# Kernel tuning notes

Hardware: AMD Instinct MI355X
Metric: run time of the kernel (lower is better)

Reference implementation:

```python
import jax, jax.numpy as jnp
import numpy as np

BATCH = 1024
INPUT_DIM = 4096
HIDDEN_DIM = 4096
N_BLOCKS = 8
BLOCK_SIZE = HIDDEN_DIM // N_BLOCKS          # 512
IN_BLOCK_SIZE = INPUT_DIM // N_BLOCKS        # 512


def setup_inputs() -> dict:
    key = jax.random.key(0)
    ks = jax.random.split(key, 6)
    scale = 1.0 / np.sqrt(BLOCK_SIZE)  # torch GRUCell init: U(-1/sqrt(hidden), 1/sqrt(hidden))
    return {
        "x": jax.random.normal(ks[0], (BATCH, INPUT_DIM), dtype=jnp.float32),
        "h": jax.random.normal(ks[1], (BATCH, HIDDEN_DIM), dtype=jnp.float32),
        "W_ih": jax.random.normal(ks[2], (N_BLOCKS, 3 * BLOCK_SIZE, IN_BLOCK_SIZE), dtype=jnp.float32) * scale,
        "W_hh": jax.random.normal(ks[3], (N_BLOCKS, 3 * BLOCK_SIZE, BLOCK_SIZE), dtype=jnp.float32) * scale,
        "b_ih": jax.random.normal(ks[4], (N_BLOCKS, 3 * BLOCK_SIZE), dtype=jnp.float32) * scale,
        "b_hh": jax.random.normal(ks[5], (N_BLOCKS, 3 * BLOCK_SIZE), dtype=jnp.float32) * scale,
    }


def reference(x, h, W_ih, W_hh, b_ih, b_hh):
    B = x.shape[0]
    n, g3, ibs = W_ih.shape           # n_blocks, 3*block_size, input_block_size
    bs = W_hh.shape[2]                # block_size
    xb = x.reshape(B, n, ibs)         # (B, n_blocks, input_block_size)
    hb = h.reshape(B, n, bs)          # (B, n_blocks, block_size)
    # Block-diagonal GEMM: one grouped matmul over all blocks at once.
    gi = jnp.einsum('bni,ngi->bng', xb, W_ih) + b_ih   # (B, n, 3*bs)
    gh = jnp.einsum('bnh,ngh->bng', hb, W_hh) + b_hh   # (B, n, 3*bs)
    i_r, i_z, i_n = jnp.split(gi, 3, axis=-1)
    h_r, h_z, h_n = jnp.split(gh, 3, axis=-1)
    r = jax.nn.sigmoid(i_r + h_r)                      # reset gate
    z = jax.nn.sigmoid(i_z + h_z)                      # update gate
    n_gate = jnp.tanh(i_n + r * h_n)                   # candidate state
    new_h = n_gate + z * (hb - n_gate)                 # torch GRUCell: h' = (1-z)*n + z*h
    return new_h.reshape(B, n * bs)
```

## Files before the change

kernel.cpp:

```cpp
#include <hip/hip_runtime.h>
#include <hip/hip_bf16.h>
#include <stdint.h>

#define G1CAST(p) ((const __attribute__((address_space(1))) void*)(p))
#define L3CAST(p) ((__attribute__((address_space(3))) void*)(p))

typedef short bf16x8 __attribute__((ext_vector_type(8)));
typedef float f32x16 __attribute__((ext_vector_type(16)));

static __device__ __forceinline__ short f2bf(float f) {
    __hip_bfloat16 b = __float2bfloat16(f);
    return __builtin_bit_cast(short, b);
}

__global__ __launch_bounds__(256) void wconv_kernel(const float* __restrict__ Wih,
                                                    const float* __restrict__ Whh,
                                                    short* __restrict__ Wstep) {
    const int b = blockIdx.x;
    const int vb = (b & 7) * 768 + (b >> 3);
    const int gid = vb * 256 + threadIdx.x;
    const int lane = gid & 63;
    int t1 = gid >> 6;
    const int g = t1 % 3;  t1 /= 3;
    const int wn = t1 & 1; t1 >>= 1;
    const int s = t1 & 63; t1 >>= 6;
    const int jt = t1 & 7;
    const int nblk = t1 >> 3;
    const int j = jt * 64 + wn * 32 + (lane & 31);
    const int kk = s * 16 + (lane >> 5) * 8;
    const float* src = (kk < 512)
        ? Wih + ((int64_t)nblk * 786432 + (int64_t)(g * 512 + j) * 512 + kk)
        : Whh + ((int64_t)nblk * 786432 + (int64_t)(g * 512 + j) * 512 + (kk - 512));
    const float4 a = ((const float4*)src)[0];
    const float4 bq = ((const float4*)src)[1];
    bf16x8 o;
    o[0] = f2bf(a.x); o[1] = f2bf(a.y); o[2] = f2bf(a.z); o[3] = f2bf(a.w);
    o[4] = f2bf(bq.x); o[5] = f2bf(bq.y); o[6] = f2bf(bq.z); o[7] = f2bf(bq.w);
    *(bf16x8*)(Wstep + (size_t)gid * 8) = o;
}

__global__ __launch_bounds__(256) void aconv_kernel(const float* __restrict__ x,
                                                    const float* __restrict__ h,
                                                    short* __restrict__ Afrag) {
    const int b = blockIdx.x;
    const int n = b & 7;
    const int inner = b >> 3;
    const int rb = inner >> 4;
    const int u = inner & 15;
    const int tid = threadIdx.x;
    const int lane = tid & 63;
    const int s = u * 4 + (tid >> 6);
    const int row = rb * 32 + (lane & 31);
    const int kk = s * 16 + (lane >> 5) * 8;
    const float* src = (kk < 512)
        ? x + ((size_t)row * 4096 + n * 512 + kk)
        : h + ((size_t)row * 4096 + n * 512 + (kk - 512));
    const float4 a = ((const float4*)src)[0];
    const float4 bq = ((const float4*)src)[1];
    bf16x8 o;
    o[0] = f2bf(a.x); o[1] = f2bf(a.y); o[2] = f2bf(a.z); o[3] = f2bf(a.w);
    o[4] = f2bf(bq.x); o[5] = f2bf(bq.y); o[6] = f2bf(bq.z); o[7] = f2bf(bq.w);
    const size_t dst = ((((size_t)(rb * 8 + n) * 64 + s) * 64) + lane) * 8;
    *(bf16x8*)(Afrag + dst) = o;
}

__global__ __launch_bounds__(256, 2) void gru_kernel(
    const float* __restrict__ hst,
    const short* __restrict__ Wstep, const short* __restrict__ Afrag,
    const float* __restrict__ b_ih, const float* __restrict__ b_hh,
    float* __restrict__ out)
{
    __shared__ __align__(16) char ldsB[6][8192];
    __shared__ __align__(16) char ldsA[6][4096];

    const int tid = threadIdx.x;
    const int nblk = blockIdx.x & 7;
    const int rr_ = blockIdx.x >> 3;
    const int bt = rr_ >> 3;
    const int jt = rr_ & 7;
    const int brow0 = bt * 128;

    const int lane = tid & 63;
    const int wave = tid >> 6;
    const int wm = wave >> 1;
    const int wn = wave & 1;
    const int l31 = lane & 31;
    const int k8 = lane >> 5;

    const int d0 = wave * 2048;
    const int ssrc0 = (d0 >= 6144) ? d0 - 6144 : d0;
    const int ssrc1 = (d0 + 1024 >= 6144) ? d0 + 1024 - 6144 : d0 + 1024;
    const char* wstep0 = (const char*)Wstep + (size_t)((nblk * 8 + jt) * 64) * 6144
                       + (size_t)lane * 16;
    const char* asrc0 = (const char*)Afrag
        + ((size_t)(((brow0 >> 5) + wave) * 8 + nblk) << 16) + (size_t)lane * 16;

    const int boff = (wn * 3) * 1024 + lane * 16;
    const int aoff = wm * 2048 + lane * 16;

    f32x16 acc_r[2] = {};
    f32x16 acc_z[2] = {};
    f32x16 acc_nx[2] = {};
    f32x16 acc_nh[2] = {};

    auto stageAB = [&](int s, int slot) {
        const int sc = s > 63 ? 63 : s;
        const char* bsrc = wstep0 + (size_t)sc * 6144;
        char* bdst = (char*)&ldsB[slot][0] + d0;
        __builtin_amdgcn_global_load_lds(G1CAST(bsrc + ssrc0), L3CAST(bdst), 16, 0, 0);
        __builtin_amdgcn_global_load_lds(G1CAST(bsrc + ssrc1), L3CAST(bdst + 1024), 16, 0, 0);
        __builtin_amdgcn_global_load_lds(G1CAST(asrc0 + (size_t)sc * 1024),
                                         L3CAST((char*)&ldsA[slot][0] + wave * 1024), 16, 0, 0);
    };

#define ITER(accN)                                                                  \
    {                                                                               \
        __builtin_amdgcn_s_barrier();                                               \
        stageAB(s_ + 5, wslot);                                                     \
        __builtin_amdgcn_sched_barrier(0);                                          \
        asm volatile("s_waitcnt vmcnt(12)" ::: "memory");                           \
        const char* bp = &ldsB[rslot][boff];                                        \
        const char* ap = &ldsA[rslot][aoff];                                        \
        bf16x8 a0v = *(const bf16x8*)(ap);                                          \
        bf16x8 a1v = *(const bf16x8*)(ap + 1024);                                   \
        bf16x8 b0 = *(const bf16x8*)(bp);                                           \
        bf16x8 b1 = *(const bf16x8*)(bp + 1024);                                    \
        bf16x8 b2 = *(const bf16x8*)(bp + 2048);                                    \
        __builtin_amdgcn_s_setprio(1);                                              \
        acc_r[0] = __builtin_amdgcn_mfma_f32_32x32x16_bf16(a0v, b0, acc_r[0], 0, 0, 0); \
        acc_r[1] = __builtin_amdgcn_mfma_f32_32x32x16_bf16(a1v, b0, acc_r[1], 0, 0, 0); \
        acc_z[0] = __builtin_amdgcn_mfma_f32_32x32x16_bf16(a0v, b1, acc_z[0], 0, 0, 0); \
        acc_z[1] = __builtin_amdgcn_mfma_f32_32x32x16_bf16(a1v, b1, acc_z[1], 0, 0, 0); \
        accN[0]  = __builtin_amdgcn_mfma_f32_32x32x16_bf16(a0v, b2, accN[0], 0, 0, 0);  \
        accN[1]  = __builtin_amdgcn_mfma_f32_32x32x16_bf16(a1v, b2, accN[1], 0, 0, 0);  \
        __builtin_amdgcn_s_setprio(0);                                              \
        rslot = (rslot == 5) ? 0 : rslot + 1;                                       \
        wslot = (wslot == 5) ? 0 : wslot + 1;                                       \
        s_ += 1;                                                                    \
    }

    stageAB(0, 0); stageAB(1, 1); stageAB(2, 2); stageAB(3, 3); stageAB(4, 4);

    int s_ = 0;
    int rslot = 0;
    int wslot = 5;

    #pragma unroll 1
    for (int g4 = 0; g4 < 8; ++g4) {
        ITER(acc_nx) ITER(acc_nx) ITER(acc_nx) ITER(acc_nx)
    }
    #pragma unroll 1
    for (int g4 = 0; g4 < 8; ++g4) {
        ITER(acc_nh) ITER(acc_nh) ITER(acc_nh) ITER(acc_nh)
    }
#undef ITER

    const int jb = jt * 64 + wn * 32 + l31;
    const int bb = nblk * 1536 + jb;
    const float br = b_ih[bb] + b_hh[bb];
    const float bz = b_ih[bb + 512] + b_hh[bb + 512];
    const float bnx = b_ih[bb + 1024];
    const float bnh = b_hh[bb + 1024];
    const int gcol = nblk * 512 + jb;
    #pragma unroll
    for (int m = 0; m < 2; ++m) {
        #pragma unroll
        for (int rr = 0; rr < 16; ++rr) {
            const int rowl = (rr & 3) + 8 * (rr >> 2) + 4 * k8;
            const int row = brow0 + wm * 64 + m * 32 + rowl;
            const size_t idx = (size_t)row * 4096 + gcol;
            const float sr = acc_r[m][rr] + br;
            const float sz = acc_z[m][rr] + bz;
            const float rg = 1.f / (1.f + __expf(-sr));
            const float zg = 1.f / (1.f + __expf(-sz));
            const float tin = (acc_nx[m][rr] + bnx) + rg * (acc_nh[m][rr] + bnh);
            const float e2 = __expf(-2.f * tin);
            const float ng = 2.f / (1.f + e2) - 1.f;
            const float hv = hst[idx];
            out[idx] = ng + zg * (hv - ng);
        }
    }
}

extern "C" void kernel_launch(void* const* d_in, const int* in_sizes, int n_in,
                              void* d_out, int out_size, void* d_ws, size_t ws_size,
                              hipStream_t stream) {
    (void)in_sizes; (void)n_in; (void)out_size; (void)ws_size;
    const float* x    = (const float*)d_in[0];
    const float* h    = (const float*)d_in[1];
    const float* W_ih = (const float*)d_in[2];
    const float* W_hh = (const float*)d_in[3];
    const float* b_ih = (const float*)d_in[4];
    const float* b_hh = (const float*)d_in[5];
    short* Wstep = (short*)d_ws;
    short* Afrag = (short*)d_ws + (size_t)12 * 1024 * 1024;

    wconv_kernel<<<6144, 256, 0, stream>>>(W_ih, W_hh, Wstep);
    aconv_kernel<<<4096, 256, 0, stream>>>(x, h, Afrag);
    gru_kernel<<<512, 256, 0, stream>>>(h, Wstep, Afrag, b_ih, b_hh, (float*)d_out);
}
```

Measured before the change: 70.72 us.

## Double block tile to 256 rows with 512 threads and coarser K stages

The GRU GEMM kernel now runs 512-thread blocks covering 256 batch rows instead of 128, so each staged weight tile is shared by twice as many rows and the grid halves to 256 blocks. The pipeline moves from a 6-slot ring with one barrier per 16-wide K step to 4 K-substeps per barrier, using double-buffered A and triple-buffered B in LDS. This cuts barrier count and weight reloads but uses about 136KB of LDS at one block per CU, and 256 blocks may leave some CUs idle.

```diff
diff --git a/kernel.cpp b/kernel.cpp
--- a/kernel.cpp
+++ b/kernel.cpp
@@ -64,21 +64,20 @@
     *(bf16x8*)(Afrag + dst) = o;
 }
 
-__global__ __launch_bounds__(256, 2) void gru_kernel(
+__global__ __launch_bounds__(512, 1) void gru_kernel(
     const float* __restrict__ hst,
     const short* __restrict__ Wstep, const short* __restrict__ Afrag,
     const float* __restrict__ b_ih, const float* __restrict__ b_hh,
     float* __restrict__ out)
 {
-    __shared__ __align__(16) char ldsB[6][8192];
-    __shared__ __align__(16) char ldsA[6][4096];
+    __shared__ __align__(16) char ldsB[3][24576];
+    __shared__ __align__(16) char ldsA[2][32768];
 
     const int tid = threadIdx.x;
     const int nblk = blockIdx.x & 7;
-    const int rr_ = blockIdx.x >> 3;
-    const int bt = rr_ >> 3;
-    const int jt = rr_ & 7;
-    const int brow0 = bt * 128;
+    const int jt = (blockIdx.x >> 3) & 7;
+    const int bt = blockIdx.x >> 6;
+    const int brow0 = bt * 256;
 
     const int lane = tid & 63;
     const int wave = tid >> 6;
@@ -87,73 +86,98 @@
     const int l31 = lane & 31;
     const int k8 = lane >> 5;
 
-    const int d0 = wave * 2048;
-    const int ssrc0 = (d0 >= 6144) ? d0 - 6144 : d0;
-    const int ssrc1 = (d0 + 1024 >= 6144) ? d0 + 1024 - 6144 : d0 + 1024;
-    const char* wstep0 = (const char*)Wstep + (size_t)((nblk * 8 + jt) * 64) * 6144
-                       + (size_t)lane * 16;
-    const char* asrc0 = (const char*)Afrag
-        + ((size_t)(((brow0 >> 5) + wave) * 8 + nblk) << 16) + (size_t)lane * 16;
-
-    const int boff = (wn * 3) * 1024 + lane * 16;
-    const int aoff = wm * 2048 + lane * 16;
+    const char* bsrc0 = (const char*)Wstep + (size_t)((nblk * 8 + jt) * 64) * 6144
+                      + (size_t)wave * 3072 + (size_t)lane * 16;
+    const int bdst0 = wave * 3072 + lane * 16;
+    size_t asrcb[4];
+    int adstb[4];
+    #pragma unroll
+    for (int o = 0; o < 4; ++o) {
+        const int c = tid + 512 * o;
+        const int rbl = c >> 8;
+        const int sub = (c >> 6) & 3;
+        const int ln = c & 63;
+        asrcb[o] = ((size_t)((bt * 8 + rbl) * 8 + nblk) << 16) + (size_t)sub * 1024 + (size_t)ln * 16;
+        adstb[o] = c * 16;
+    }
+
+    const int boffr = (wn * 3) * 1024 + lane * 16;
+    const int aoffr0 = (2 * wm) * 4096 + lane * 16;
+    const int aoffr1 = (2 * wm + 1) * 4096 + lane * 16;
 
     f32x16 acc_r[2] = {};
     f32x16 acc_z[2] = {};
     f32x16 acc_nx[2] = {};
     f32x16 acc_nh[2] = {};
 
-    auto stageAB = [&](int s, int slot) {
-        const int sc = s > 63 ? 63 : s;
-        const char* bsrc = wstep0 + (size_t)sc * 6144;
-        char* bdst = (char*)&ldsB[slot][0] + d0;
-        __builtin_amdgcn_global_load_lds(G1CAST(bsrc + ssrc0), L3CAST(bdst), 16, 0, 0);
-        __builtin_amdgcn_global_load_lds(G1CAST(bsrc + ssrc1), L3CAST(bdst + 1024), 16, 0, 0);
-        __builtin_amdgcn_global_load_lds(G1CAST(asrc0 + (size_t)sc * 1024),
-                                         L3CAST((char*)&ldsA[slot][0] + wave * 1024), 16, 0, 0);
+    auto stageA = [&](int it, int slot) {
+        const int ic = it > 15 ? 15 : it;
+        char* dst = (char*)&ldsA[slot][0];
+        #pragma unroll
+        for (int o = 0; o < 4; ++o)
+            __builtin_amdgcn_global_load_lds(G1CAST((const char*)Afrag + asrcb[o] + (size_t)ic * 4096),
+                                             L3CAST(dst + adstb[o]), 16, 0, 0);
     };
-
-#define ITER(accN)                                                                  \
+    auto stageB = [&](int it, int slot) {
+        const int ic = it > 15 ? 15 : it;
+        const char* src = bsrc0 + (size_t)ic * 24576;
+        char* dst = (char*)&ldsB[slot][0] + bdst0;
+        #pragma unroll
+        for (int o = 0; o < 3; ++o)
+            __builtin_amdgcn_global_load_lds(G1CAST(src + o * 1024),
+                                             L3CAST(dst + o * 1024), 16, 0, 0);
+    };
+
+#define SUBSTEP(u, accN)                                                            \
     {                                                                               \
-        __builtin_amdgcn_s_barrier();                                               \
-        stageAB(s_ + 5, wslot);                                                     \
-        __builtin_amdgcn_sched_barrier(0);                                          \
-        asm volatile("s_waitcnt vmcnt(12)" ::: "memory");                           \
-        const char* bp = &ldsB[rslot][boff];                                        \
-        const char* ap = &ldsA[rslot][aoff];                                        \
-        bf16x8 a0v = *(const bf16x8*)(ap);                                          \
-        bf16x8 a1v = *(const bf16x8*)(ap + 1024);                                   \
+        const char* bp = (const char*)&ldsB[rslot][0] + (u) * 6144 + boffr;         \
+        const char* ap = (const char*)&ldsA[i_ & 1][0] + (u) * 1024;                \
+        bf16x8 a0 = *(const bf16x8*)(ap + aoffr0);                                  \
+        bf16x8 a1 = *(const bf16x8*)(ap + aoffr1);                                  \
         bf16x8 b0 = *(const bf16x8*)(bp);                                           \
         bf16x8 b1 = *(const bf16x8*)(bp + 1024);                                    \
         bf16x8 b2 = *(const bf16x8*)(bp + 2048);                                    \
-        __builtin_amdgcn_s_setprio(1);                                              \
-        acc_r[0] = __builtin_amdgcn_mfma_f32_32x32x16_bf16(a0v, b0, acc_r[0], 0, 0, 0); \
-        acc_r[1] = __builtin_amdgcn_mfma_f32_32x32x16_bf16(a1v, b0, acc_r[1], 0, 0, 0); \
-        acc_z[0] = __builtin_amdgcn_mfma_f32_32x32x16_bf16(a0v, b1, acc_z[0], 0, 0, 0); \
-        acc_z[1] = __builtin_amdgcn_mfma_f32_32x32x16_bf16(a1v, b1, acc_z[1], 0, 0, 0); \
-        accN[0]  = __builtin_amdgcn_mfma_f32_32x32x16_bf16(a0v, b2, accN[0], 0, 0, 0);  \
-        accN[1]  = __builtin_amdgcn_mfma_f32_32x32x16_bf16(a1v, b2, accN[1], 0, 0, 0);  \
-        __builtin_amdgcn_s_setprio(0);                                              \
-        rslot = (rslot == 5) ? 0 : rslot + 1;                                       \
-        wslot = (wslot == 5) ? 0 : wslot + 1;                                       \
-        s_ += 1;                                                                    \
-    }
-
-    stageAB(0, 0); stageAB(1, 1); stageAB(2, 2); stageAB(3, 3); stageAB(4, 4);
-
-    int s_ = 0;
+        acc_r[0] = __builtin_amdgcn_mfma_f32_32x32x16_bf16(a0, b0, acc_r[0], 0, 0, 0); \
+        acc_r[1] = __builtin_amdgcn_mfma_f32_32x32x16_bf16(a1, b0, acc_r[1], 0, 0, 0); \
+        acc_z[0] = __builtin_amdgcn_mfma_f32_32x32x16_bf16(a0, b1, acc_z[0], 0, 0, 0); \
+        acc_z[1] = __builtin_amdgcn_mfma_f32_32x32x16_bf16(a1, b1, acc_z[1], 0, 0, 0); \
+        accN[0]  = __builtin_amdgcn_mfma_f32_32x32x16_bf16(a0, b2, accN[0], 0, 0, 0);  \
+        accN[1]  = __builtin_amdgcn_mfma_f32_32x32x16_bf16(a1, b2, accN[1], 0, 0, 0);  \
+    }
+
+#define ITER(accN)                                                                  \
+    {                                                                               \
+        asm volatile("s_waitcnt vmcnt(3)" ::: "memory");                            \
+        __builtin_amdgcn_s_barrier();                                               \
+        stageA(i_ + 1, (i_ + 1) & 1);                                               \
+        stageB(i_ + 2, stslot);                                                     \
+        SUBSTEP(0, accN)                                                            \
+        SUBSTEP(1, accN)                                                            \
+        SUBSTEP(2, accN)                                                            \
+        SUBSTEP(3, accN)                                                            \
+        rslot = (rslot == 2) ? 0 : rslot + 1;                                       \
+        stslot = (stslot == 2) ? 0 : stslot + 1;                                    \
+        i_ += 1;                                                                    \
+    }
+
+    stageB(0, 0);
+    stageA(0, 0);
+    stageB(1, 1);
+
+    int i_ = 0;
     int rslot = 0;
-    int wslot = 5;
+    int stslot = 2;
 
     #pragma unroll 1
-    for (int g4 = 0; g4 < 8; ++g4) {
-        ITER(acc_nx) ITER(acc_nx) ITER(acc_nx) ITER(acc_nx)
+    for (int g2 = 0; g2 < 8; ++g2) {
+        ITER(acc_nx)
     }
     #pragma unroll 1
-    for (int g4 = 0; g4 < 8; ++g4) {
-        ITER(acc_nh) ITER(acc_nh) ITER(acc_nh) ITER(acc_nh)
+    for (int g2 = 0; g2 < 8; ++g2) {
+        ITER(acc_nh)
     }
 #undef ITER
+#undef SUBSTEP
 
     const int jb = jt * 64 + wn * 32 + l31;
     const int bb = nblk * 1536 + jb;
@@ -197,5 +221,5 @@
 
     wconv_kernel<<<6144, 256, 0, stream>>>(W_ih, W_hh, Wstep);
     aconv_kernel<<<4096, 256, 0, stream>>>(x, h, Afrag);
-    gru_kernel<<<512, 256, 0, stream>>>(h, Wstep, Afrag, b_ih, b_hh, (float*)d_out);
-}
+    gru_kernel<<<256, 512, 0, stream>>>(h, Wstep, Afrag, b_ih, b_hh, (float*)d_out);
+}
```

After: 62.68 us. 11.4% less time.
